# Performance work log

Hardware: AMD Instinct MI355X
Metric: run time of the kernel (lower is better)

Reference implementation:

```python
import jax, jax.numpy as jnp
import numpy as np

B, N, C, H = 8, 1024, 512, 8
EPS = 1e-6


def setup_inputs() -> dict:
    key = jax.random.key(0)
    k0, k1, k2, k3, k4 = jax.random.split(key, 5)
    x = jax.random.normal(k0, (B, N, C), dtype=jnp.float32)
    # nonnegative random-walk visit-frequency mask stand-in
    mask = jax.random.uniform(k1, (N, N), dtype=jnp.float32)
    w_qkv = jax.random.normal(k2, (C, 3 * C), dtype=jnp.float32) * 0.02
    w_out = jax.random.normal(k3, (C, C), dtype=jnp.float32) * 0.02
    b_out = jax.random.normal(k4, (C,), dtype=jnp.float32) * 0.02
    return {"x": x, "mask": mask, "w_qkv": w_qkv, "w_out": w_out, "b_out": b_out}


def reference(x, mask, w_qkv, w_out, b_out):
    b, n, c = x.shape
    d = c // H
    qkv = x @ w_qkv                                   # [B,N,3C]
    q, k, v = jnp.split(qkv, 3, axis=-1)

    def to_heads(t):
        return t.reshape(b, n, H, d).transpose(0, 2, 1, 3)  # [B,H,N,D]

    q, k, v = to_heads(q), to_heads(k), to_heads(v)
    # positive feature map
    q = jax.nn.relu(q) + EPS
    k = jax.nn.relu(k) + EPS
    # graph diffusion: (q^T @ mask)^T == einsum over source node m
    q = q + 0.1 * jnp.einsum('bhmd,mn->bhnd', q, mask)
    k = k + 0.1 * jnp.einsum('bhmd,mn->bhnd', k, mask)
    # linear kernel scores, elementwise-masked
    kernel = jnp.einsum('bhnd,bhmd->bhnm', q, k) * mask   # [B,H,N,N]
    z = 1.0 / (kernel.sum(axis=-1, keepdims=True) + EPS)  # [B,H,N,1]
    out = jnp.einsum('bhnm,bhmd->bhnd', kernel, v) * z    # [B,H,N,D]
    out = out.transpose(0, 2, 1, 3).reshape(b, n, c)      # [B,N,C]
    return out @ w_out + b_out
```

## Files before the change

kernel.cpp:

```cpp
#include <hip/hip_runtime.h>
#include <cstddef>

#define Bsz 8
#define Nn  1024
#define Cc  512
#define Hh  8
#define Dd  64
#define EPSF 1e-6f

typedef __attribute__((ext_vector_type(8))) short short8;
typedef __attribute__((ext_vector_type(4))) float floatx4;

static __device__ __forceinline__ short f2bf(float f) {
    union { float f; unsigned u; } v; v.f = f;
    unsigned r = (v.u + 0x7FFFu + ((v.u >> 16) & 1u)) >> 16;
    return (short)r;
}
static __device__ __forceinline__ float bf2f(short s) {
    union { unsigned u; float f; } v; v.u = ((unsigned)(unsigned short)s) << 16;
    return v.f;
}

#define GLOAD_LDS16(gp, lp)                                              \
    __builtin_amdgcn_global_load_lds(                                    \
        (const __attribute__((address_space(1))) void*)(gp),             \
        (__attribute__((address_space(3))) void*)(lp), 16, 0, 0)

static __device__ __forceinline__
void stage_tile(short* __restrict__ lds, const short* __restrict__ src,
                int ldsrc, int tid, int CHUNKS, int SLOTS) {
    #pragma unroll
    for (int s = tid; s < SLOTS; s += 256) {
        int r = s / CHUNKS, cs = s % CHUNKS;
        int gc = cs ^ (r & 7);
        GLOAD_LDS16(&src[(size_t)r * ldsrc + gc * 8], &lds[s * 8]);
    }
}
static __device__ __forceinline__
short8 fragT(const short* __restrict__ lds, int CHUNKS, int r, int lc) {
    return *(const short8*)&lds[(r * CHUNKS + (lc ^ (r & 7))) * 8];
}

__global__ __launch_bounds__(256)
void prep_all(const float* __restrict__ x, const float* __restrict__ mask,
              const float* __restrict__ wq, const float* __restrict__ wo,
              short* __restrict__ xb, short* __restrict__ Ad,
              short* __restrict__ wqT, short* __restrict__ woT,
              short* __restrict__ mbf) {
    __shared__ float t[64][65];
    const int tid = threadIdx.x;
    const int bid = blockIdx.x;

    if (bid < 2048) {
        int idx = bid * 256 + tid;
        const float* s = &x[(size_t)idx * 8];
        union { short h[8]; int4 v; } u;
        #pragma unroll
        for (int j = 0; j < 8; j++) u.h[j] = f2bf(s[j]);
        *(int4*)&xb[(size_t)idx * 8] = u.v;
        return;
    }
    if (bid < 2304) {
        int idx = bid - 2048;
        const int n0 = (idx & 15) * 64, m0 = (idx >> 4) * 64;
        #pragma unroll
        for (int i = 0; i < 4; i++) {
            int k = i * 256 + tid;
            int r = k >> 4, c4 = (k & 15) * 4;
            *(float4*)&t[r][c4] = *(const float4*)&mask[(size_t)(m0 + r) * Nn + n0 + c4];
        }
        __syncthreads();
        #pragma unroll
        for (int i = 0; i < 4; i++) {
            int k = i * 256 + tid;
            int rr = k >> 4, c4 = (k & 15) * 4;
            union { short h[4]; int2 v; } u;
            #pragma unroll
            for (int j = 0; j < 4; j++) {
                int mm = c4 + j;
                float v = 0.1f * t[mm][rr] + ((n0 + rr) == (m0 + mm) ? 1.0f : 0.0f);
                u.h[j] = f2bf(v);
            }
            *(int2*)&Ad[(size_t)(n0 + rr) * Nn + m0 + c4] = u.v;
        }
        return;
    }
    if (bid < 2496) {
        int idx = bid - 2304;
        const int n0 = (idx % 24) * 64, k0 = (idx / 24) * 64;
        #pragma unroll
        for (int i = 0; i < 4; i++) {
            int k = i * 256 + tid;
            int r = k >> 4, c4 = (k & 15) * 4;
            *(float4*)&t[r][c4] = *(const float4*)&wq[(size_t)(k0 + r) * 1536 + n0 + c4];
        }
        __syncthreads();
        #pragma unroll
        for (int i = 0; i < 4; i++) {
            int k = i * 256 + tid;
            int rr = k >> 4, c4 = (k & 15) * 4;
            union { short h[4]; int2 v; } u;
            #pragma unroll
            for (int j = 0; j < 4; j++) u.h[j] = f2bf(t[c4 + j][rr]);
            *(int2*)&wqT[(size_t)(n0 + rr) * 512 + k0 + c4] = u.v;
        }
        return;
    }
    if (bid < 2560) {
        int idx = bid - 2496;
        const int n0 = (idx & 7) * 64, k0 = (idx >> 3) * 64;
        #pragma unroll
        for (int i = 0; i < 4; i++) {
            int k = i * 256 + tid;
            int r = k >> 4, c4 = (k & 15) * 4;
            *(float4*)&t[r][c4] = *(const float4*)&wo[(size_t)(k0 + r) * 512 + n0 + c4];
        }
        __syncthreads();
        #pragma unroll
        for (int i = 0; i < 4; i++) {
            int k = i * 256 + tid;
            int rr = k >> 4, c4 = (k & 15) * 4;
            union { short h[4]; int2 v; } u;
            #pragma unroll
            for (int j = 0; j < 4; j++) u.h[j] = f2bf(t[c4 + j][rr]);
            *(int2*)&woT[(size_t)(n0 + rr) * 512 + k0 + c4] = u.v;
        }
        return;
    }
    {
        int idx = (bid - 2560) * 256 + tid;
        const float* s = &mask[(size_t)idx * 8];
        union { short h[8]; int4 v; } u;
        #pragma unroll
        for (int j = 0; j < 8; j++) u.h[j] = f2bf(s[j]);
        *(int4*)&mbf[(size_t)idx * 8] = u.v;
    }
}

__global__ __launch_bounds__(256)
void gemm_qkv(const short* __restrict__ xb, const short* __restrict__ wqT,
              short* __restrict__ qT, short* __restrict__ kT,
              short* __restrict__ vT) {
    __shared__ short smem[17408];
    short* As = smem;
    short* Bs = smem + 8192;

    const int tid = threadIdx.x;
    const int m0 = blockIdx.x * 128;
    const int n0 = blockIdx.y * 128;
    const int wave = tid >> 6, lane = tid & 63;
    const int quad = lane >> 4, l16 = lane & 15;
    const int wm = (wave >> 1) * 64, wn = (wave & 1) * 64;

    floatx4 acc[4][4];
    #pragma unroll
    for (int i = 0; i < 4; i++)
        #pragma unroll
        for (int j = 0; j < 4; j++) acc[i][j] = (floatx4){0.f, 0.f, 0.f, 0.f};

    const short* Ab = xb  + (size_t)m0 * 512;
    const short* Bb = wqT + (size_t)n0 * 512;

    for (int k0 = 0; k0 < 512; k0 += 64) {
        __syncthreads();
        stage_tile(As, Ab + k0, 512, tid, 8, 1024);
        stage_tile(Bs, Bb + k0, 512, tid, 8, 1024);
        __syncthreads();
        #pragma unroll
        for (int kh = 0; kh < 2; kh++) {
            short8 a[4], b[4];
            #pragma unroll
            for (int i = 0; i < 4; i++) a[i] = fragT(As, 8, wm + i * 16 + l16, kh * 4 + quad);
            #pragma unroll
            for (int i = 0; i < 4; i++) b[i] = fragT(Bs, 8, wn + i * 16 + l16, kh * 4 + quad);
            #pragma unroll
            for (int mi = 0; mi < 4; mi++)
                #pragma unroll
                for (int ni = 0; ni < 4; ni++)
                    acc[mi][ni] = __builtin_amdgcn_mfma_f32_16x16x32_bf16(
                        a[mi], b[ni], acc[mi][ni], 0, 0, 0);
        }
    }

    __syncthreads();
    short* Tt = smem;
    const int doRelu = (n0 < 1024);
    #pragma unroll
    for (int mi = 0; mi < 4; mi++)
        #pragma unroll
        for (int ni = 0; ni < 4; ni++)
            #pragma unroll
            for (int r = 0; r < 4; r++) {
                float v = acc[mi][ni][r];
                if (doRelu) v = fmaxf(v, 0.0f) + EPSF;
                int nl = wn + ni * 16 + l16;
                int ml = wm + mi * 16 + quad * 4 + r;
                Tt[nl * 136 + ml] = f2bf(v);
            }
    __syncthreads();

    const int b = m0 >> 10, m_in = m0 & 1023;
    int row = tid >> 1, half = tid & 1;
    int cg = n0 + row;
    int part = cg >> 9, ci = cg & 511;
    short* base = (part == 0) ? qT : (part == 1) ? kT : vT;
    short* dst = base + ((size_t)b * 512 + ci) * 1024 + m_in + half * 64;
    const short* srcl = &Tt[row * 136 + half * 64];
    #pragma unroll
    for (int i = 0; i < 8; i++)
        *(int4*)&dst[i * 8] = *(const int4*)&srcl[i * 8];
}

__global__ __launch_bounds__(256)
void gemm_diff(const short* __restrict__ Ad, const short* __restrict__ qT,
               const short* __restrict__ kT, short* __restrict__ qd,
               short* __restrict__ kd) {
    __shared__ short smem[16384];
    short* As = smem;
    short* Bs = smem + 8192;

    const int tid = threadIdx.x;
    const int z = blockIdx.x, b = z >> 1, part = z & 1;
    const short* BTb = (part ? kT : qT) + (size_t)b * 512 * 1024;
    short* outb = (part ? kd : qd) + (size_t)b * 1024 * 512;

    const int c0 = blockIdx.y * 128;
    const int r0 = blockIdx.z * 128;
    const int wave = tid >> 6, lane = tid & 63;
    const int quad = lane >> 4, l16 = lane & 15;
    const int wm = (wave >> 1) * 64, wn = (wave & 1) * 64;

    floatx4 acc[4][4];
    #pragma unroll
    for (int i = 0; i < 4; i++)
        #pragma unroll
        for (int j = 0; j < 4; j++) acc[i][j] = (floatx4){0.f, 0.f, 0.f, 0.f};

    const short* Ab = Ad  + (size_t)r0 * 1024;
    const short* Bb = BTb + (size_t)c0 * 1024;

    for (int k0 = 0; k0 < 1024; k0 += 64) {
        __syncthreads();
        stage_tile(As, Ab + k0, 1024, tid, 8, 1024);
        stage_tile(Bs, Bb + k0, 1024, tid, 8, 1024);
        __syncthreads();
        #pragma unroll
        for (int kh = 0; kh < 2; kh++) {
            short8 a[4], b2[4];
            #pragma unroll
            for (int i = 0; i < 4; i++) a[i]  = fragT(As, 8, wm + i * 16 + l16, kh * 4 + quad);
            #pragma unroll
            for (int i = 0; i < 4; i++) b2[i] = fragT(Bs, 8, wn + i * 16 + l16, kh * 4 + quad);
            #pragma unroll
            for (int mi = 0; mi < 4; mi++)
                #pragma unroll
                for (int ni = 0; ni < 4; ni++)
                    acc[mi][ni] = __builtin_amdgcn_mfma_f32_16x16x32_bf16(
                        a[mi], b2[ni], acc[mi][ni], 0, 0, 0);
        }
    }

    #pragma unroll
    for (int mi = 0; mi < 4; mi++)
        #pragma unroll
        for (int r = 0; r < 4; r++) {
            int n = r0 + wm + mi * 16 + quad * 4 + r;
            #pragma unroll
            for (int ni = 0; ni < 4; ni++) {
                int c = c0 + wn + ni * 16 + l16;
                outb[(size_t)n * 512 + c] = f2bf(acc[mi][ni][r]);
            }
        }
}

__global__ __launch_bounds__(256)
void attn_mfma(const short* __restrict__ qd, const short* __restrict__ kd,
               const short* __restrict__ vTg, const short* __restrict__ mbf,
               short* __restrict__ abf) {
    __shared__ short qs[8192];
    __shared__ short ks[4096];
    __shared__ short vt[4096];
    __shared__ short ss[8192];
    __shared__ short ms[8192];

    const int tid = threadIdx.x;
    const int bh = blockIdx.x;
    const int b = bh >> 3, h = bh & 7;
    const int n0 = blockIdx.y * 128;

    const int wave = tid >> 6, lane = tid & 63;
    const int quad = lane >> 4, l16 = lane & 15;

    const short* Qb = qd + ((size_t)b * Nn + n0) * Cc + h * Dd;
    const short* Kb = kd + (size_t)b * Nn * Cc + h * Dd;
    const short* Vb = vTg + ((size_t)b * Cc + h * Dd) * Nn;
    const short* Mb = mbf + (size_t)n0 * Nn;

    stage_tile(qs, Qb, Cc, tid, 8, 1024);
    __syncthreads();
    short8 aT[2][2];
    #pragma unroll
    for (int t = 0; t < 2; t++) {
        aT[t][0] = fragT(qs, 8, wave * 32 + t * 16 + l16, quad);
        aT[t][1] = fragT(qs, 8, wave * 32 + t * 16 + l16, 4 + quad);
    }

    float dreg[2] = {0.f, 0.f};
    floatx4 nacc[2][4];
    #pragma unroll
    for (int t = 0; t < 2; t++)
        #pragma unroll
        for (int i = 0; i < 4; i++) nacc[t][i] = (floatx4){0.f, 0.f, 0.f, 0.f};

    const int ssrow[2] = { wave * 32 + l16, wave * 32 + 16 + l16 };

    for (int m0 = 0; m0 < Nn; m0 += 64) {
        __syncthreads();
        stage_tile(ks, Kb + (size_t)m0 * Cc, Cc, tid, 8, 512);
        stage_tile(vt, Vb + m0, Nn, tid, 8, 512);
        stage_tile(ms, Mb + m0, Nn, tid, 8, 1024);
        __syncthreads();

        #pragma unroll
        for (int mt = 0; mt < 4; mt++) {
            const short8 k0f = fragT(ks, 8, mt * 16 + l16, quad);
            const short8 k1f = fragT(ks, 8, mt * 16 + l16, 4 + quad);
            #pragma unroll
            for (int t = 0; t < 2; t++) {
                floatx4 s = (floatx4){0.f, 0.f, 0.f, 0.f};
                s = __builtin_amdgcn_mfma_f32_16x16x32_bf16(k0f, aT[t][0], s, 0, 0, 0);
                s = __builtin_amdgcn_mfma_f32_16x16x32_bf16(k1f, aT[t][1], s, 0, 0, 0);
                const int row = ssrow[t];
                const int c = mt * 16 + quad * 4;
                const int off = (row * 8 + ((c >> 3) ^ (row & 7))) * 8 + (c & 7);
                union { short h[4]; int2 v; } mk;
                mk.v = *(const int2*)&ms[off];
                float sv0 = s[0] * bf2f(mk.h[0]);
                float sv1 = s[1] * bf2f(mk.h[1]);
                float sv2 = s[2] * bf2f(mk.h[2]);
                float sv3 = s[3] * bf2f(mk.h[3]);
                dreg[t] += (sv0 + sv1) + (sv2 + sv3);
                union { short h[4]; int2 v; } pk;
                pk.h[0] = f2bf(sv0); pk.h[1] = f2bf(sv1);
                pk.h[2] = f2bf(sv2); pk.h[3] = f2bf(sv3);
                *(int2*)&ss[off] = pk.v;
            }
        }

        short8 p[2][2];
        #pragma unroll
        for (int t = 0; t < 2; t++) {
            p[t][0] = fragT(ss, 8, wave * 32 + t * 16 + l16, quad);
            p[t][1] = fragT(ss, 8, wave * 32 + t * 16 + l16, 4 + quad);
        }
        #pragma unroll
        for (int dt = 0; dt < 4; dt++) {
            const short8 v0 = fragT(vt, 8, dt * 16 + l16, quad);
            const short8 v1 = fragT(vt, 8, dt * 16 + l16, 4 + quad);
            #pragma unroll
            for (int t = 0; t < 2; t++) {
                nacc[t][dt] = __builtin_amdgcn_mfma_f32_16x16x32_bf16(p[t][0], v0, nacc[t][dt], 0, 0, 0);
                nacc[t][dt] = __builtin_amdgcn_mfma_f32_16x16x32_bf16(p[t][1], v1, nacc[t][dt], 0, 0, 0);
            }
        }
    }

    #pragma unroll
    for (int t = 0; t < 2; t++) {
        dreg[t] += __shfl_xor(dreg[t], 16, 64);
        dreg[t] += __shfl_xor(dreg[t], 32, 64);
    }

    #pragma unroll
    for (int t = 0; t < 2; t++)
        #pragma unroll
        for (int r = 0; r < 4; r++) {
            int nloc = quad * 4 + r;
            float den = __shfl(dreg[t], nloc, 64);
            int n = n0 + wave * 32 + t * 16 + nloc;
            float zr = 1.0f / (den + EPSF);
            #pragma unroll
            for (int dt = 0; dt < 4; dt++) {
                size_t o = ((size_t)b * Nn + n) * Cc + h * Dd + dt * 16 + l16;
                abf[o] = f2bf(nacc[t][dt][r] * zr);
            }
        }
}

__global__ __launch_bounds__(256)
void gemm_out(const short* __restrict__ abf, const short* __restrict__ woT,
              const float* __restrict__ bias, float* __restrict__ out) {
    __shared__ short smem[12288];
    short* As = smem;
    short* Bs = smem + 4096;

    const int tid = threadIdx.x;
    const int m0 = blockIdx.y * 64;
    const int n0 = blockIdx.x * 128;
    const int wave = tid >> 6, lane = tid & 63;
    const int quad = lane >> 4, l16 = lane & 15;
    const int wm = (wave >> 1) * 32, wn = (wave & 1) * 64;

    floatx4 acc[2][4];
    #pragma unroll
    for (int i = 0; i < 2; i++)
        #pragma unroll
        for (int j = 0; j < 4; j++) acc[i][j] = (floatx4){0.f, 0.f, 0.f, 0.f};

    const short* Ab = abf + (size_t)m0 * 512;
    const short* Bb = woT + (size_t)n0 * 512;

    for (int k0 = 0; k0 < 512; k0 += 64) {
        __syncthreads();
        stage_tile(As, Ab + k0, 512, tid, 8, 512);
        stage_tile(Bs, Bb + k0, 512, tid, 8, 1024);
        __syncthreads();
        #pragma unroll
        for (int kh = 0; kh < 2; kh++) {
            short8 a[2], b[4];
            #pragma unroll
            for (int i = 0; i < 2; i++)
                a[i] = fragT(As, 8, wm + i * 16 + l16, kh * 4 + quad);
            #pragma unroll
            for (int i = 0; i < 4; i++)
                b[i] = fragT(Bs, 8, wn + i * 16 + l16, kh * 4 + quad);
            #pragma unroll
            for (int mi = 0; mi < 2; mi++)
                #pragma unroll
                for (int ni = 0; ni < 4; ni++)
                    acc[mi][ni] = __builtin_amdgcn_mfma_f32_16x16x32_bf16(
                        a[mi], b[ni], acc[mi][ni], 0, 0, 0);
        }
    }

    #pragma unroll
    for (int mi = 0; mi < 2; mi++)
        #pragma unroll
        for (int r = 0; r < 4; r++) {
            int m = m0 + wm + mi * 16 + quad * 4 + r;
            #pragma unroll
            for (int ni = 0; ni < 4; ni++) {
                int n = n0 + wn + ni * 16 + l16;
                out[(size_t)m * 512 + n] = acc[mi][ni][r] + bias[n];
            }
        }
}

extern "C" void kernel_launch(void* const* d_in, const int* in_sizes, int n_in,
                              void* d_out, int out_size, void* d_ws, size_t ws_size,
                              hipStream_t stream) {
    const float* x     = (const float*)d_in[0];
    const float* mask  = (const float*)d_in[1];
    const float* w_qkv = (const float*)d_in[2];
    const float* w_out = (const float*)d_in[3];
    const float* b_out = (const float*)d_in[4];
    float* out = (float*)d_out;

    char* p = (char*)d_ws;
    short* xb  = (short*)p; p += 8388608;
    short* wqT = (short*)p; p += 1572864;
    short* Ad  = (short*)p; p += 2097152;
    short* woT = (short*)p; p += 524288;
    short* mbf = (short*)p; p += 2097152;
    short* qT  = (short*)p; p += 8388608;
    short* kT  = (short*)p; p += 8388608;
    short* vT  = (short*)p; p += 8388608;
    short* qd  = (short*)p; p += 8388608;
    short* kd  = (short*)p; p += 8388608;
    short* abf = (short*)p; p += 8388608;

    dim3 blk(256);

    prep_all  <<<3072, blk, 0, stream>>>(x, mask, w_qkv, w_out,
                                         xb, Ad, wqT, woT, mbf);
    gemm_qkv  <<<dim3(64, 12), blk, 0, stream>>>(xb, wqT, qT, kT, vT);
    gemm_diff <<<dim3(16, 4, 8), blk, 0, stream>>>(Ad, qT, kT, qd, kd);
    attn_mfma <<<dim3(64, 8),  blk, 0, stream>>>(qd, kd, vT, mbf, abf);
    gemm_out  <<<dim3(4, 128), blk, 0, stream>>>(abf, woT, b_out, out);
}
```

Before: 167.7 us.

## Rewrite QKV GEMM as 256x256 double-buffered 8-wave pipelined kernel

The QKV projection GEMM now uses 256x256 output tiles with 512 threads, 128 KB of dynamic LDS holding double-buffered A and B tiles, and a staged schedule. That schedule issues async global->LDS loads for the next K tile between MFMA phases, with raw barriers, vmcnt waits and s_setprio. The grid is remapped so blocks are spread across XCDs, and the epilogue transposes through a per-wave swizzled LDS tile. The aim is to hide global load latency and raise MFMA utilisation compared with the single-buffered 128x128 version. In exchange it uses heavy LDS and registers and has only 192 blocks, so occupancy may be low. The hand-placed waitcnt and barriers must also be exactly right to avoid races.

```diff
diff --git a/kernel.cpp b/kernel.cpp
--- a/kernel.cpp
+++ b/kernel.cpp
@@ -40,6 +40,10 @@
 short8 fragT(const short* __restrict__ lds, int CHUNKS, int r, int lc) {
     return *(const short8*)&lds[(r * CHUNKS + (lc ^ (r & 7))) * 8];
 }
+
+#define FENCE() asm volatile("" ::: "memory")
+#define BARRIER_RAW() do { FENCE(); __builtin_amdgcn_s_barrier(); FENCE(); } while (0)
+#define WAITVM(N) asm volatile("s_waitcnt vmcnt(" #N ")" ::: "memory")
 
 __global__ __launch_bounds__(256)
 void prep_all(const float* __restrict__ x, const float* __restrict__ mask,
@@ -137,78 +141,173 @@
     }
 }
 
-__global__ __launch_bounds__(256)
+static __device__ __forceinline__
+void stageA_half(short* __restrict__ buf, const short* __restrict__ gA,
+                 int kt, int h, int tid) {
+    #pragma unroll
+    for (int kk = 0; kk < 2; kk++) {
+        int i = tid + kk * 512;
+        int run = i >> 9;
+        int within = i & 511;
+        int r = run * 128 + h * 64 + (within >> 3);
+        int c = within & 7;
+        int gc = c ^ (r & 7);
+        GLOAD_LDS16(gA + (size_t)r * 512 + kt + gc * 8, buf + (r * 8 + c) * 8);
+    }
+}
+static __device__ __forceinline__
+void stageB_half(short* __restrict__ buf, const short* __restrict__ gB,
+                 int kt, int h, int tid) {
+    #pragma unroll
+    for (int kk = 0; kk < 2; kk++) {
+        int i = tid + kk * 512;
+        int run = i >> 8;
+        int within = i & 255;
+        int r = run * 64 + h * 32 + (within >> 3);
+        int c = within & 7;
+        int gc = c ^ (r & 7);
+        GLOAD_LDS16(gB + (size_t)r * 512 + kt + gc * 8, buf + (r * 8 + c) * 8);
+    }
+}
+
+template<int MH>
+static __device__ __forceinline__
+void readA8(const short* __restrict__ bufA, short8 (&aF)[4][2],
+            int wr, int l16, int quad) {
+    #pragma unroll
+    for (int f = 0; f < 4; f++)
+        #pragma unroll
+        for (int kk = 0; kk < 2; kk++)
+            aF[f][kk] = fragT(bufA, 8, wr * 128 + MH * 64 + f * 16 + l16, kk * 4 + quad);
+}
+template<int NH>
+static __device__ __forceinline__
+void readB4(const short* __restrict__ bufB, short8 (&bF)[2][2],
+            int wc, int l16, int quad) {
+    #pragma unroll
+    for (int g = 0; g < 2; g++)
+        #pragma unroll
+        for (int kk = 0; kk < 2; kk++)
+            bF[g][kk] = fragT(bufB, 8, wc * 64 + NH * 32 + g * 16 + l16, kk * 4 + quad);
+}
+template<int MH, int NH>
+static __device__ __forceinline__
+void mfma16(short8 (&aF)[4][2], short8 (&bF)[2][2], floatx4 (&acc)[8][4]) {
+    #pragma unroll
+    for (int kk = 0; kk < 2; kk++)
+        #pragma unroll
+        for (int f = 0; f < 4; f++)
+            #pragma unroll
+            for (int g = 0; g < 2; g++)
+                acc[MH * 4 + f][NH * 2 + g] = __builtin_amdgcn_mfma_f32_16x16x32_bf16(
+                    aF[f][kk], bF[g][kk], acc[MH * 4 + f][NH * 2 + g], 0, 0, 0);
+}
+
+__global__ __launch_bounds__(512, 2)
 void gemm_qkv(const short* __restrict__ xb, const short* __restrict__ wqT,
               short* __restrict__ qT, short* __restrict__ kT,
               short* __restrict__ vT) {
-    __shared__ short smem[17408];
-    short* As = smem;
-    short* Bs = smem + 8192;
+    extern __shared__ short smem[];
 
     const int tid = threadIdx.x;
-    const int m0 = blockIdx.x * 128;
-    const int n0 = blockIdx.y * 128;
-    const int wave = tid >> 6, lane = tid & 63;
+    const int lin = blockIdx.x;
+    const int wgid = (lin & 7) * 24 + (lin >> 3);
+    const int mt = wgid / 6, nt = wgid % 6;
+    const int m0 = mt * 256, n0 = nt * 256;
+
+    const int wid = tid >> 6, lane = tid & 63;
     const int quad = lane >> 4, l16 = lane & 15;
-    const int wm = (wave >> 1) * 64, wn = (wave & 1) * 64;
-
-    floatx4 acc[4][4];
-    #pragma unroll
-    for (int i = 0; i < 4; i++)
-        #pragma unroll
-        for (int j = 0; j < 4; j++) acc[i][j] = (floatx4){0.f, 0.f, 0.f, 0.f};
+    const int wr = wid >> 2, wc = wid & 3;
 
     const short* Ab = xb  + (size_t)m0 * 512;
     const short* Bb = wqT + (size_t)n0 * 512;
 
-    for (int k0 = 0; k0 < 512; k0 += 64) {
-        __syncthreads();
-        stage_tile(As, Ab + k0, 512, tid, 8, 1024);
-        stage_tile(Bs, Bb + k0, 512, tid, 8, 1024);
-        __syncthreads();
-        #pragma unroll
-        for (int kh = 0; kh < 2; kh++) {
-            short8 a[4], b[4];
-            #pragma unroll
-            for (int i = 0; i < 4; i++) a[i] = fragT(As, 8, wm + i * 16 + l16, kh * 4 + quad);
-            #pragma unroll
-            for (int i = 0; i < 4; i++) b[i] = fragT(Bs, 8, wn + i * 16 + l16, kh * 4 + quad);
-            #pragma unroll
-            for (int mi = 0; mi < 4; mi++)
-                #pragma unroll
-                for (int ni = 0; ni < 4; ni++)
-                    acc[mi][ni] = __builtin_amdgcn_mfma_f32_16x16x32_bf16(
-                        a[mi], b[ni], acc[mi][ni], 0, 0, 0);
-        }
-    }
-
-    __syncthreads();
-    short* Tt = smem;
+    floatx4 acc[8][4];
+    #pragma unroll
+    for (int i = 0; i < 8; i++)
+        #pragma unroll
+        for (int j = 0; j < 4; j++) acc[i][j] = (floatx4){0.f, 0.f, 0.f, 0.f};
+
+    short8 aF[4][2], bF[2][2];
+
+    stageA_half(smem,          Ab, 0, 0, tid);
+    stageB_half(smem + 16384,  Bb, 0, 0, tid);
+    stageA_half(smem,          Ab, 0, 1, tid);
+    stageB_half(smem + 16384,  Bb, 0, 1, tid);
+    WAITVM(4); BARRIER_RAW();
+
+    for (int j = 0; j < 8; ++j) {
+        const short* cA = smem + (j & 1) * 32768;
+        const short* cB = cA + 16384;
+        short* nA = smem + ((j + 1) & 1) * 32768;
+        short* nB = nA + 16384;
+        const int kn = ((j + 1) & 7) * 64;
+
+        readA8<0>(cA, aF, wr, l16, quad);
+        readB4<0>(cB, bF, wc, l16, quad);
+        stageA_half(nA, Ab, kn, 0, tid);
+        stageB_half(nB, Bb, kn, 0, tid);
+        BARRIER_RAW();
+        __builtin_amdgcn_s_setprio(1);
+        mfma16<0, 0>(aF, bF, acc);
+        __builtin_amdgcn_s_setprio(0);
+        WAITVM(4); BARRIER_RAW();
+
+        readA8<1>(cA, aF, wr, l16, quad);
+        stageA_half(nA, Ab, kn, 1, tid);
+        stageB_half(nB, Bb, kn, 1, tid);
+        BARRIER_RAW();
+        __builtin_amdgcn_s_setprio(1);
+        mfma16<1, 0>(aF, bF, acc);
+        __builtin_amdgcn_s_setprio(0);
+        BARRIER_RAW();
+
+        readB4<1>(cB, bF, wc, l16, quad);
+        BARRIER_RAW();
+        __builtin_amdgcn_s_setprio(1);
+        mfma16<1, 1>(aF, bF, acc);
+        __builtin_amdgcn_s_setprio(0);
+        BARRIER_RAW();
+
+        readA8<0>(cA, aF, wr, l16, quad);
+        BARRIER_RAW();
+        __builtin_amdgcn_s_setprio(1);
+        mfma16<0, 1>(aF, bF, acc);
+        __builtin_amdgcn_s_setprio(0);
+        WAITVM(4); BARRIER_RAW();
+    }
+
+    WAITVM(0); BARRIER_RAW();
+
+    short* T = smem + wid * 8192;
     const int doRelu = (n0 < 1024);
     #pragma unroll
-    for (int mi = 0; mi < 4; mi++)
-        #pragma unroll
-        for (int ni = 0; ni < 4; ni++)
-            #pragma unroll
-            for (int r = 0; r < 4; r++) {
-                float v = acc[mi][ni][r];
+    for (int mf = 0; mf < 8; mf++)
+        #pragma unroll
+        for (int nf = 0; nf < 4; nf++)
+            #pragma unroll
+            for (int rr = 0; rr < 4; rr++) {
+                float v = acc[mf][nf][rr];
                 if (doRelu) v = fmaxf(v, 0.0f) + EPSF;
-                int nl = wn + ni * 16 + l16;
-                int ml = wm + mi * 16 + quad * 4 + r;
-                Tt[nl * 136 + ml] = f2bf(v);
-            }
-    __syncthreads();
-
-    const int b = m0 >> 10, m_in = m0 & 1023;
-    int row = tid >> 1, half = tid & 1;
-    int cg = n0 + row;
-    int part = cg >> 9, ci = cg & 511;
-    short* base = (part == 0) ? qT : (part == 1) ? kT : vT;
-    short* dst = base + ((size_t)b * 512 + ci) * 1024 + m_in + half * 64;
-    const short* srcl = &Tt[row * 136 + half * 64];
-    #pragma unroll
-    for (int i = 0; i < 8; i++)
-        *(int4*)&dst[i * 8] = *(const int4*)&srcl[i * 8];
+                int row = nf * 16 + l16;
+                int col = mf * 16 + quad * 4 + rr;
+                T[row * 128 + (col ^ ((row & 15) << 3))] = f2bf(v);
+            }
+    const int gm0 = m0 + wr * 128;
+    const int b = gm0 >> 10, m_in0 = gm0 & 1023;
+    #pragma unroll
+    for (int g = 0; g < 4; g++) {
+        int row = (lane >> 2) + g * 16;
+        int gn = n0 + wc * 64 + row;
+        int part = gn >> 9, ci = gn & 511;
+        short* base = (part == 0) ? qT : (part == 1) ? kT : vT;
+        short* dst = base + ((size_t)b * 512 + ci) * 1024 + m_in0;
+        #pragma unroll
+        for (int cc = 0; cc < 4; cc++) {
+            int cs = ((lane & 3) + cc * 4) * 8;
+            *(int4*)&dst[cs] = *(const int4*)&T[row * 128 + (cs ^ ((row & 15) << 3))];
+        }
+    }
 }
 
 __global__ __launch_bounds__(256)
@@ -469,11 +568,18 @@
     short* kd  = (short*)p; p += 8388608;
     short* abf = (short*)p; p += 8388608;
 
+    static int attr_set = 0;
+    if (!attr_set) {
+        hipFuncSetAttribute(reinterpret_cast<const void*>(gemm_qkv),
+                            hipFuncAttributeMaxDynamicSharedMemorySize, 131072);
+        attr_set = 1;
+    }
+
     dim3 blk(256);
 
     prep_all  <<<3072, blk, 0, stream>>>(x, mask, w_qkv, w_out,
                                          xb, Ad, wqT, woT, mbf);
-    gemm_qkv  <<<dim3(64, 12), blk, 0, stream>>>(xb, wqT, qT, kT, vT);
+    gemm_qkv  <<<dim3(192), dim3(512), 131072, stream>>>(xb, wqT, qT, kT, vT);
     gemm_diff <<<dim3(16, 4, 8), blk, 0, stream>>>(Ad, qT, kT, qd, kd);
     attn_mfma <<<dim3(64, 8),  blk, 0, stream>>>(qd, kd, vT, mbf, abf);
     gemm_out  <<<dim3(4, 128), blk, 0, stream>>>(abf, woT, b_out, out);
```

Measured after the change: 165.9 us. Within noise of the previous version (-1.1%).
